# Kernel tuning notes

Measured on AMD Instinct MI355X. Metric: run time of the kernel, lower is better.

Reference implementation:

```python
import jax, jax.numpy as jnp
import numpy as np

N = 100000   # nodes (polyline vectors)
E = 800000   # directed edges (intra-polyline, avg degree 8)
NC = 10000   # clusters (polylines)
C0 = 64      # in_channels
H = 64       # hidden_unit
L = 3        # num_subgraph_layres
LN_EPS = 1e-5


def setup_inputs() -> dict:
    key = jax.random.key(0)
    ks = jax.random.split(key, 4 + 2 * L)
    d = {}
    d["x"] = jax.random.normal(ks[0], (N, C0), jnp.float32)
    d["edge_index"] = jax.random.randint(ks[1], (2, E), 0, N, dtype=jnp.int32)
    d["cluster"] = jax.random.randint(ks[2], (N,), 0, NC, dtype=jnp.int32)
    c = C0
    for i in range(L):
        k1, k2 = jax.random.split(ks[3 + i], 2)
        d[f"W1_{i}"] = jax.random.normal(k1, (c, H), jnp.float32) * (1.0 / np.sqrt(c))
        d[f"b1_{i}"] = jnp.zeros((H,), jnp.float32)
        d[f"g_{i}"] = jnp.ones((H,), jnp.float32)
        d[f"be_{i}"] = jnp.zeros((H,), jnp.float32)
        d[f"W2_{i}"] = jax.random.normal(k2, (H, c), jnp.float32) * (1.0 / np.sqrt(H))
        d[f"b2_{i}"] = jnp.zeros((c,), jnp.float32)
        c *= 2
    return d


def _glp_layer(x, edge_index, W1, b1, g, be, W2, b2):
    # MLP: Linear -> LayerNorm -> ReLU -> Linear
    h = x @ W1 + b1                                   # [N, H]
    mu = h.mean(axis=-1, keepdims=True)
    var = ((h - mu) ** 2).mean(axis=-1, keepdims=True)
    h = (h - mu) * jax.lax.rsqrt(var + LN_EPS) * g + be
    h = jax.nn.relu(h)
    h = h @ W2 + b2                                   # [N, C]
    # message = x_j (source features), aggr='max' at target nodes
    msg = h[edge_index[0]]                            # [E, C] gather
    aggr = jax.ops.segment_max(msg, edge_index[1], num_segments=h.shape[0])
    aggr = jnp.where(jnp.isfinite(aggr), aggr, 0.0)   # nodes with no in-edges -> 0
    # update: concat([x, aggr_out]) -> channels double
    return jnp.concatenate([h, aggr], axis=1)


def reference(x, edge_index, cluster,
              W1_0, b1_0, g_0, be_0, W2_0, b2_0,
              W1_1, b1_1, g_1, be_1, W2_1, b2_1,
              W1_2, b1_2, g_2, be_2, W2_2, b2_2):
    params = [
        (W1_0, b1_0, g_0, be_0, W2_0, b2_0),
        (W1_1, b1_1, g_1, be_1, W2_1, b2_1),
        (W1_2, b1_2, g_2, be_2, W2_2, b2_2),
    ]
    for p in params:
        x = _glp_layer(x, edge_index, *p)
    # max_pool over clusters (per-polyline max)
    pooled = jax.ops.segment_max(x, cluster, num_segments=NC)  # [NC, 8*C0]
    pooled = jnp.where(jnp.isfinite(pooled), pooled, 0.0)
    # column-wise L2 normalization: out.x / out.x.norm(dim=0)
    return pooled / jnp.linalg.norm(pooled, axis=0)
```

## Files before the change

### kernel.cpp

```cpp
#include <hip/hip_runtime.h>
#include <hip/hip_bf16.h>

#define NN 100000
#define NE 800000
#define NCL 10000
#define CAPN 32
#define CAPC 40

typedef __attribute__((ext_vector_type(8))) short short8;
typedef __attribute__((ext_vector_type(4))) float f32x4;

__device__ __forceinline__ float bflo(unsigned int u) {
  return __uint_as_float(u << 16);
}
__device__ __forceinline__ float bfhi(unsigned int u) {
  return __uint_as_float(u & 0xffff0000u);
}
__device__ __forceinline__ unsigned short f2bf(float f) {
  unsigned int u = __float_as_uint(f);
  u += 0x7fffu + ((u >> 16) & 1u);
  return (unsigned short)(u >> 16);
}
__device__ __forceinline__ unsigned int packbf_exact(float lo, float hi) {
  return (__float_as_uint(lo) >> 16) | (__float_as_uint(hi) & 0xffff0000u);
}

struct WtDesc { const float* src; unsigned short* dst; int rows, cols; };
struct WtPack { WtDesc d[6]; };
__global__ __launch_bounds__(256) void prep_kernel(int* zbase, int zn, int zblocks, WtPack p) {
  if ((int)blockIdx.x < zblocks) {
    int i = blockIdx.x * 256 + threadIdx.x;
    if (i < zn) zbase[i] = 0;
    return;
  }
  int b = blockIdx.x - zblocks;
  const long stride = 32L * 256;
  for (int a = 0; a < 6; ++a) {
    int rows = p.d[a].rows, cols = p.d[a].cols, n = rows * cols;
    const float* src = p.d[a].src;
    unsigned short* dst = p.d[a].dst;
    for (long i = (long)b * 256 + threadIdx.x; i < n; i += stride) {
      int r = (int)(i / cols), c = (int)(i % cols);
      dst[(long)c * rows + r] = f2bf(src[(long)r * cols + c]);
    }
  }
}

__device__ __forceinline__ void scatter_body(
    int i,
    const int* __restrict__ ei, int* __restrict__ cnt, int* __restrict__ bucket,
    const int* __restrict__ cl, int* __restrict__ ccnt, int* __restrict__ cbucket) {
  if (i < NE / 4) {
    int4 t = reinterpret_cast<const int4*>(ei + NE)[i];
    int4 s = reinterpret_cast<const int4*>(ei)[i];
    int p0 = atomicAdd(&cnt[t.x], 1);
    int p1 = atomicAdd(&cnt[t.y], 1);
    int p2 = atomicAdd(&cnt[t.z], 1);
    int p3 = atomicAdd(&cnt[t.w], 1);
    if (p0 < CAPN) bucket[t.x * CAPN + p0] = s.x;
    if (p1 < CAPN) bucket[t.y * CAPN + p1] = s.y;
    if (p2 < CAPN) bucket[t.z * CAPN + p2] = s.z;
    if (p3 < CAPN) bucket[t.w * CAPN + p3] = s.w;
  } else if (i < NE / 4 + NN / 4) {
    int j = i - NE / 4;
    int4 c = reinterpret_cast<const int4*>(cl)[j];
    int n0 = j * 4;
    int p0 = atomicAdd(&ccnt[c.x], 1);
    int p1 = atomicAdd(&ccnt[c.y], 1);
    int p2 = atomicAdd(&ccnt[c.z], 1);
    int p3 = atomicAdd(&ccnt[c.w], 1);
    if (p0 < CAPC) cbucket[c.x * CAPC + p0] = n0;
    if (p1 < CAPC) cbucket[c.y * CAPC + p1] = n0 + 1;
    if (p2 < CAPC) cbucket[c.z * CAPC + p2] = n0 + 2;
    if (p3 < CAPC) cbucket[c.w * CAPC + p3] = n0 + 3;
  }
}

template<int C, bool INF32, bool DO_SCATTER>
__global__ __launch_bounds__(256) void mlp_mfma_kernel(
    const void* __restrict__ xin_v,
    const unsigned short* __restrict__ W1T,
    const float* __restrict__ b1, const float* __restrict__ g, const float* __restrict__ be,
    const unsigned short* __restrict__ W2T,
    const float* __restrict__ b2,
    unsigned short* __restrict__ out, int outstride, int ntiles,
    int sblocks,
    const int* __restrict__ ei, int* __restrict__ cnt, int* __restrict__ bucket,
    const int* __restrict__ cl, int* __restrict__ ccnt, int* __restrict__ cbucket)
{
  constexpr int CP = C + 8;
  __shared__ unsigned short w1s[64 * CP];
  __shared__ unsigned short w2s[C * 72];
  __shared__ unsigned short ps[4 * 16 * 72];
  int tid = threadIdx.x;

  if constexpr (DO_SCATTER) {
    if ((int)blockIdx.x < sblocks) {
      scatter_body(blockIdx.x * 256 + tid, ei, cnt, bucket, cl, ccnt, cbucket);
      return;
    }
  }
  int bid = blockIdx.x - (DO_SCATTER ? sblocks : 0);
  int mgrid = gridDim.x - (DO_SCATTER ? sblocks : 0);

  for (int i = tid; i < 64 * (C / 8); i += 256) {
    int r = i / (C / 8), cc = i % (C / 8);
    *reinterpret_cast<uint4*>(&w1s[r * CP + cc * 8]) =
        *reinterpret_cast<const uint4*>(W1T + r * C + cc * 8);
  }
  for (int i = tid; i < C * 8; i += 256) {
    int r = i / 8, cc = i % 8;
    *reinterpret_cast<uint4*>(&w2s[r * 72 + cc * 8]) =
        *reinterpret_cast<const uint4*>(W2T + r * 64 + cc * 8);
  }
  __syncthreads();

  int wv = tid >> 6, lane = tid & 63;
  int l15 = lane & 15, q = lane >> 4;
  unsigned short* psw = &ps[wv * 16 * 72];

  float b1v[4], gv[4], bev[4];
  #pragma unroll
  for (int t = 0; t < 4; ++t) {
    b1v[t] = b1[t * 16 + l15];
    gv[t]  = g[t * 16 + l15];
    bev[t] = be[t * 16 + l15];
  }
  constexpr int NT2 = C / 16;
  float b2v[NT2];
  #pragma unroll
  for (int tc = 0; tc < NT2; ++tc) b2v[tc] = b2[tc * 16 + l15];

  for (long tile = (long)bid * 4 + wv; tile < ntiles; tile += (long)mgrid * 4) {
    long nb = tile * 16;
    long arow = nb + l15;

    f32x4 acc[4];
    #pragma unroll
    for (int t = 0; t < 4; ++t) acc[t] = (f32x4){0.f, 0.f, 0.f, 0.f};
    #pragma unroll
    for (int kk = 0; kk < C / 32; ++kk) {
      short8 a;
      if constexpr (INF32) {
        const float* xf = (const float*)xin_v;
        const float* src = xf + arow * C + kk * 32 + q * 8;
        float4 v0 = reinterpret_cast<const float4*>(src)[0];
        float4 v1 = reinterpret_cast<const float4*>(src)[1];
        a[0] = (short)f2bf(v0.x); a[1] = (short)f2bf(v0.y);
        a[2] = (short)f2bf(v0.z); a[3] = (short)f2bf(v0.w);
        a[4] = (short)f2bf(v1.x); a[5] = (short)f2bf(v1.y);
        a[6] = (short)f2bf(v1.z); a[7] = (short)f2bf(v1.w);
      } else {
        const unsigned short* xh = (const unsigned short*)xin_v;
        a = *reinterpret_cast<const short8*>(xh + arow * C + kk * 32 + q * 8);
      }
      #pragma unroll
      for (int t = 0; t < 4; ++t) {
        short8 b = *reinterpret_cast<const short8*>(&w1s[(t * 16 + l15) * CP + kk * 32 + q * 8]);
        acc[t] = __builtin_amdgcn_mfma_f32_16x16x32_bf16(a, b, acc[t], 0, 0, 0);
      }
    }

    float vout[4][4];
    #pragma unroll
    for (int r = 0; r < 4; ++r) {
      float h0 = acc[0][r] + b1v[0];
      float h1 = acc[1][r] + b1v[1];
      float h2 = acc[2][r] + b1v[2];
      float h3 = acc[3][r] + b1v[3];
      float s = (h0 + h1) + (h2 + h3);
      s += __shfl_xor(s, 1); s += __shfl_xor(s, 2);
      s += __shfl_xor(s, 4); s += __shfl_xor(s, 8);
      float mu = s * (1.0f / 64.0f);
      float d0 = h0 - mu, d1 = h1 - mu, d2 = h2 - mu, d3 = h3 - mu;
      float qs = (d0 * d0 + d1 * d1) + (d2 * d2 + d3 * d3);
      qs += __shfl_xor(qs, 1); qs += __shfl_xor(qs, 2);
      qs += __shfl_xor(qs, 4); qs += __shfl_xor(qs, 8);
      float rinv = rsqrtf(qs * (1.0f / 64.0f) + 1e-5f);
      vout[0][r] = fmaxf(0.f, d0 * rinv * gv[0] + bev[0]);
      vout[1][r] = fmaxf(0.f, d1 * rinv * gv[1] + bev[1]);
      vout[2][r] = fmaxf(0.f, d2 * rinv * gv[2] + bev[2]);
      vout[3][r] = fmaxf(0.f, d3 * rinv * gv[3] + bev[3]);
    }

    #pragma unroll
    for (int t = 0; t < 4; ++t)
      #pragma unroll
      for (int r = 0; r < 4; ++r)
        psw[(q * 4 + r) * 72 + t * 16 + l15] = f2bf(vout[t][r]);

    short8 a0 = *reinterpret_cast<const short8*>(&psw[l15 * 72 + q * 8]);
    short8 a1 = *reinterpret_cast<const short8*>(&psw[l15 * 72 + 32 + q * 8]);
    long node0 = nb + q * 4;
    #pragma unroll
    for (int tc = 0; tc < NT2; ++tc) {
      short8 b0 = *reinterpret_cast<const short8*>(&w2s[(tc * 16 + l15) * 72 + q * 8]);
      short8 b1w = *reinterpret_cast<const short8*>(&w2s[(tc * 16 + l15) * 72 + 32 + q * 8]);
      f32x4 c = (f32x4){0.f, 0.f, 0.f, 0.f};
      c = __builtin_amdgcn_mfma_f32_16x16x32_bf16(a0, b0, c, 0, 0, 0);
      c = __builtin_amdgcn_mfma_f32_16x16x32_bf16(a1, b1w, c, 0, 0, 0);
      #pragma unroll
      for (int r = 0; r < 4; ++r)
        out[(node0 + r) * (long)outstride + tc * 16 + l15] = f2bf(c[r] + b2v[tc]);
    }
  }
}

template<int C>
__global__ __launch_bounds__(256) void aggr_kernel(
    const int* __restrict__ cnt, const int* __restrict__ bucket,
    unsigned short* __restrict__ xnext)
{
  constexpr int Q = C / 8;
  constexpr int NPB = 256 / Q;
  int q = threadIdx.x & (Q - 1);
  int ln = threadIdx.x / Q;
  long node = (long)blockIdx.x * NPB + ln;
  int end = min(cnt[node], CAPN);
  const int* bl = bucket + node * CAPN;
  float m[8];
  #pragma unroll
  for (int k = 0; k < 8; ++k) m[k] = -3.4e38f;

  auto acc8 = [&](uint4 u) {
    m[0] = fmaxf(m[0], bflo(u.x)); m[1] = fmaxf(m[1], bfhi(u.x));
    m[2] = fmaxf(m[2], bflo(u.y)); m[3] = fmaxf(m[3], bfhi(u.y));
    m[4] = fmaxf(m[4], bflo(u.z)); m[5] = fmaxf(m[5], bfhi(u.z));
    m[6] = fmaxf(m[6], bflo(u.w)); m[7] = fmaxf(m[7], bfhi(u.w));
  };
  auto row = [&](int s) {
    return reinterpret_cast<const uint4*>(xnext + (long)s * (2 * C))[q];
  };

  int e = 0;
  for (; e + 3 < end; e += 4) {
    int s0 = bl[e], s1 = bl[e + 1], s2 = bl[e + 2], s3 = bl[e + 3];
    uint4 u0 = row(s0), u1 = row(s1), u2 = row(s2), u3 = row(s3);
    acc8(u0); acc8(u1); acc8(u2); acc8(u3);
  }
  for (; e < end; ++e) acc8(row(bl[e]));
  if (end == 0) {
    #pragma unroll
    for (int k = 0; k < 8; ++k) m[k] = 0.f;
  }
  uint4 o;
  o.x = packbf_exact(m[0], m[1]);
  o.y = packbf_exact(m[2], m[3]);
  o.z = packbf_exact(m[4], m[5]);
  o.w = packbf_exact(m[6], m[7]);
  reinterpret_cast<uint4*>(xnext + (long)node * (2 * C) + C)[q] = o;
}

__global__ __launch_bounds__(256) void pool_kernel(
    const int* __restrict__ ccnt, const int* __restrict__ cbucket,
    const unsigned short* __restrict__ x3, float* __restrict__ pooled)
{
  int q = threadIdx.x & 63;
  int lc = threadIdx.x >> 6;
  long k = (long)blockIdx.x * 4 + lc;
  int end = min(ccnt[k], CAPC);
  const int* bl = cbucket + k * CAPC;
  float m[8];
  #pragma unroll
  for (int t = 0; t < 8; ++t) m[t] = -3.4e38f;

  auto acc8 = [&](uint4 u) {
    m[0] = fmaxf(m[0], bflo(u.x)); m[1] = fmaxf(m[1], bfhi(u.x));
    m[2] = fmaxf(m[2], bflo(u.y)); m[3] = fmaxf(m[3], bfhi(u.y));
    m[4] = fmaxf(m[4], bflo(u.z)); m[5] = fmaxf(m[5], bfhi(u.z));
    m[6] = fmaxf(m[6], bflo(u.w)); m[7] = fmaxf(m[7], bfhi(u.w));
  };
  auto row = [&](int n) {
    return reinterpret_cast<const uint4*>(x3 + (long)n * 512)[q];
  };

  int e = 0;
  for (; e + 3 < end; e += 4) {
    int n0 = bl[e], n1 = bl[e + 1], n2 = bl[e + 2], n3 = bl[e + 3];
    uint4 u0 = row(n0), u1 = row(n1), u2 = row(n2), u3 = row(n3);
    acc8(u0); acc8(u1); acc8(u2); acc8(u3);
  }
  for (; e < end; ++e) acc8(row(bl[e]));
  if (end == 0) {
    #pragma unroll
    for (int t = 0; t < 8; ++t) m[t] = 0.f;
  }
  float* orow = pooled + k * 512 + q * 8;
  reinterpret_cast<float4*>(orow)[0] = make_float4(m[0], m[1], m[2], m[3]);
  reinterpret_cast<float4*>(orow)[1] = make_float4(m[4], m[5], m[6], m[7]);
}

__global__ __launch_bounds__(256) void colnorm_kernel(const float* __restrict__ pooled,
                                                      float* __restrict__ normsq) {
  int tid = threadIdx.x;
  int rows_per = (NCL + gridDim.x - 1) / gridDim.x;
  int r0 = blockIdx.x * rows_per;
  int r1 = min(r0 + rows_per, NCL);
  float s0 = 0.f, s1 = 0.f;
  for (int r = r0; r < r1; ++r) {
    float a = pooled[(long)r * 512 + tid];
    float b = pooled[(long)r * 512 + 256 + tid];
    s0 = fmaf(a, a, s0);
    s1 = fmaf(b, b, s1);
  }
  atomicAdd(&normsq[tid], s0);
  atomicAdd(&normsq[tid + 256], s1);
}

__global__ __launch_bounds__(256) void normalize_kernel(const float* __restrict__ pooled,
                                                        const float* __restrict__ normsq,
                                                        float* __restrict__ out) {
  long idx = (long)blockIdx.x * 256 + threadIdx.x;
  if (idx < (long)NCL * 512) {
    float nv = normsq[idx & 511];
    out[idx] = pooled[idx] * rsqrtf(nv);
  }
}

extern "C" void kernel_launch(void* const* d_in, const int* in_sizes, int n_in,
                              void* d_out, int out_size, void* d_ws, size_t ws_size,
                              hipStream_t stream) {
  const float* x0 = (const float*)d_in[0];
  const int* ei = (const int*)d_in[1];
  const int* cl = (const int*)d_in[2];

  const float* W1f[3]; const float* b1f[3]; const float* gf[3];
  const float* bef[3]; const float* W2f[3]; const float* b2f[3];
  for (int i = 0; i < 3; ++i) {
    W1f[i] = (const float*)d_in[3 + 6 * i + 0];
    b1f[i] = (const float*)d_in[3 + 6 * i + 1];
    gf[i]  = (const float*)d_in[3 + 6 * i + 2];
    bef[i] = (const float*)d_in[3 + 6 * i + 3];
    W2f[i] = (const float*)d_in[3 + 6 * i + 4];
    b2f[i] = (const float*)d_in[3 + 6 * i + 5];
  }

  char* ws = (char*)d_ws;
  size_t off = 0;
  auto take = [&](size_t bytes) {
    size_t o = off; off = (off + bytes + 255) & ~(size_t)255; return o;
  };
  unsigned short* x3 = (unsigned short*)(ws + take((size_t)NN * 512 * 2));
  unsigned short* x1 = x3;
  unsigned short* x2 = (unsigned short*)(ws + take((size_t)NN * 256 * 2));
  size_t szBucket = (size_t)NN * CAPN * 4;
  size_t szPooled = (size_t)NCL * 512 * 4;
  size_t regA = take(szBucket > szPooled ? szBucket : szPooled);
  int* bucket = (int*)(ws + regA);
  float* pooled = (float*)(ws + regA);
  int* cbucket = (int*)(ws + take((size_t)NCL * CAPC * 4));
  int* zero_base = (int*)(ws + take((size_t)(NN + NCL + 512) * 4));
  int* cnt = zero_base;
  int* ccnt = zero_base + NN;
  float* normsq = (float*)(zero_base + NN + NCL);

  int Cs[3] = {64, 128, 256};
  unsigned short *W1T[3], *W2T[3];
  for (int i = 0; i < 3; ++i) {
    W1T[i] = (unsigned short*)(ws + take((size_t)64 * Cs[i] * 2));
    W2T[i] = (unsigned short*)(ws + take((size_t)Cs[i] * 64 * 2));
  }

  if (off > ws_size) return;

  WtPack wp;
  for (int i = 0; i < 3; ++i) {
    wp.d[2 * i + 0] = { W1f[i], W1T[i], Cs[i], 64 };
    wp.d[2 * i + 1] = { W2f[i], W2T[i], 64, Cs[i] };
  }

  int zn = NN + NCL + 512;
  int zblocks = (zn + 255) / 256;
  prep_kernel<<<zblocks + 32, 256, 0, stream>>>(zero_base, zn, zblocks, wp);

  int ntiles = NN / 16;
  int nblk = (ntiles / 2 + 3) / 4;
  int nwork = NE / 4 + NN / 4;
  int sblocks = (nwork + 255) / 256;

  mlp_mfma_kernel<64, true, true><<<sblocks + nblk, 256, 0, stream>>>(
      x0, W1T[0], b1f[0], gf[0], bef[0], W2T[0], b2f[0], x1, 128, ntiles,
      sblocks, ei, cnt, bucket, cl, ccnt, cbucket);
  aggr_kernel<64><<<NN / 32, 256, 0, stream>>>(cnt, bucket, x1);
  mlp_mfma_kernel<128, false, false><<<nblk, 256, 0, stream>>>(
      x1, W1T[1], b1f[1], gf[1], bef[1], W2T[1], b2f[1], x2, 256, ntiles,
      0, nullptr, nullptr, nullptr, nullptr, nullptr, nullptr);
  aggr_kernel<128><<<NN / 16, 256, 0, stream>>>(cnt, bucket, x2);
  mlp_mfma_kernel<256, false, false><<<nblk, 256, 0, stream>>>(
      x2, W1T[2], b1f[2], gf[2], bef[2], W2T[2], b2f[2], x3, 512, ntiles,
      0, nullptr, nullptr, nullptr, nullptr, nullptr, nullptr);
  aggr_kernel<256><<<NN / 8, 256, 0, stream>>>(cnt, bucket, x3);

  pool_kernel<<<NCL / 4, 256, 0, stream>>>(ccnt, cbucket, x3, pooled);
  colnorm_kernel<<<128, 256, 0, stream>>>(pooled, normsq);
  normalize_kernel<<<((long)NCL * 512 + 255) / 256, 256, 0, stream>>>(pooled, normsq, (float*)d_out);
}
```

Baseline: 411.1 us.

## Fuse last-layer edge max-aggregation into cluster pooling kernel

The final layer's neighbor max-aggregation is no longer materialized. The pooling kernel now computes, for each node in a cluster, its max over in-neighbors on the fly and folds it into the right half of the pooled output, while the left half takes the node's own features. This removes the 512-wide x3 write plus its re-read and drops one kernel launch. In exchange the same neighbor gathers run inside a serial per-cluster loop with 32 lanes per cluster, which may lower memory-level parallelism, and the workspace buffers are now aliased differently.

```diff
diff --git a/kernel.cpp b/kernel.cpp
--- a/kernel.cpp
+++ b/kernel.cpp
@@ -251,43 +251,63 @@
   reinterpret_cast<uint4*>(xnext + (long)node * (2 * C) + C)[q] = o;
 }
 
-__global__ __launch_bounds__(256) void pool_kernel(
+__global__ __launch_bounds__(256) void poolfuse_kernel(
     const int* __restrict__ ccnt, const int* __restrict__ cbucket,
-    const unsigned short* __restrict__ x3, float* __restrict__ pooled)
+    const int* __restrict__ cnt, const int* __restrict__ bucket,
+    const unsigned short* __restrict__ h3, float* __restrict__ pooled)
 {
-  int q = threadIdx.x & 63;
-  int lc = threadIdx.x >> 6;
-  long k = (long)blockIdx.x * 4 + lc;
-  int end = min(ccnt[k], CAPC);
-  const int* bl = cbucket + k * CAPC;
-  float m[8];
+  int q = threadIdx.x & 31;
+  int lc = threadIdx.x >> 5;
+  long k = (long)blockIdx.x * 8 + lc;
+  int cend = min(ccnt[k], CAPC);
+  const int* cbl = cbucket + k * CAPC;
+
+  float mL[8], mR[8];
   #pragma unroll
-  for (int t = 0; t < 8; ++t) m[t] = -3.4e38f;
-
-  auto acc8 = [&](uint4 u) {
+  for (int t = 0; t < 8; ++t) { mL[t] = -3.4e38f; mR[t] = -3.4e38f; }
+
+  auto fold = [](float* m, uint4 u) {
     m[0] = fmaxf(m[0], bflo(u.x)); m[1] = fmaxf(m[1], bfhi(u.x));
     m[2] = fmaxf(m[2], bflo(u.y)); m[3] = fmaxf(m[3], bfhi(u.y));
     m[4] = fmaxf(m[4], bflo(u.z)); m[5] = fmaxf(m[5], bfhi(u.z));
     m[6] = fmaxf(m[6], bflo(u.w)); m[7] = fmaxf(m[7], bfhi(u.w));
   };
   auto row = [&](int n) {
-    return reinterpret_cast<const uint4*>(x3 + (long)n * 512)[q];
+    return reinterpret_cast<const uint4*>(h3 + (long)n * 256)[q];
   };
 
-  int e = 0;
-  for (; e + 3 < end; e += 4) {
-    int n0 = bl[e], n1 = bl[e + 1], n2 = bl[e + 2], n3 = bl[e + 3];
-    uint4 u0 = row(n0), u1 = row(n1), u2 = row(n2), u3 = row(n3);
-    acc8(u0); acc8(u1); acc8(u2); acc8(u3);
-  }
-  for (; e < end; ++e) acc8(row(bl[e]));
-  if (end == 0) {
-    #pragma unroll
-    for (int t = 0; t < 8; ++t) m[t] = 0.f;
-  }
-  float* orow = pooled + k * 512 + q * 8;
-  reinterpret_cast<float4*>(orow)[0] = make_float4(m[0], m[1], m[2], m[3]);
-  reinterpret_cast<float4*>(orow)[1] = make_float4(m[4], m[5], m[6], m[7]);
+  for (int i = 0; i < cend; ++i) {
+    int n = cbl[i];
+    fold(mL, row(n));
+    int ee = min(cnt[n], CAPN);
+    const int* bl = bucket + (long)n * CAPN;
+    float nm[8];
+    #pragma unroll
+    for (int t = 0; t < 8; ++t) nm[t] = -3.4e38f;
+    int e = 0;
+    for (; e + 3 < ee; e += 4) {
+      int s0 = bl[e], s1 = bl[e + 1], s2 = bl[e + 2], s3 = bl[e + 3];
+      uint4 u0 = row(s0), u1 = row(s1), u2 = row(s2), u3 = row(s3);
+      fold(nm, u0); fold(nm, u1); fold(nm, u2); fold(nm, u3);
+    }
+    for (; e < ee; ++e) fold(nm, row(bl[e]));
+    if (ee == 0) {
+      #pragma unroll
+      for (int t = 0; t < 8; ++t) nm[t] = 0.f;
+    }
+    #pragma unroll
+    for (int t = 0; t < 8; ++t) mR[t] = fmaxf(mR[t], nm[t]);
+  }
+  if (cend == 0) {
+    #pragma unroll
+    for (int t = 0; t < 8; ++t) { mL[t] = 0.f; mR[t] = 0.f; }
+  }
+  float* oL = pooled + k * 512 + q * 8;
+  float* oR = oL + 256;
+  reinterpret_cast<float4*>(oL)[0] = make_float4(mL[0], mL[1], mL[2], mL[3]);
+  reinterpret_cast<float4*>(oL)[1] = make_float4(mL[4], mL[5], mL[6], mL[7]);
+  reinterpret_cast<float4*>(oR)[0] = make_float4(mR[0], mR[1], mR[2], mR[3]);
+  reinterpret_cast<float4*>(oR)[1] = make_float4(mR[4], mR[5], mR[6], mR[7]);
 }
 
 __global__ __launch_bounds__(256) void colnorm_kernel(const float* __restrict__ pooled,
@@ -340,14 +360,11 @@
   auto take = [&](size_t bytes) {
     size_t o = off; off = (off + bytes + 255) & ~(size_t)255; return o;
   };
-  unsigned short* x3 = (unsigned short*)(ws + take((size_t)NN * 512 * 2));
-  unsigned short* x1 = x3;
+  unsigned short* x1 = (unsigned short*)(ws + take((size_t)NN * 256 * 2));
+  unsigned short* x3c = x1;
   unsigned short* x2 = (unsigned short*)(ws + take((size_t)NN * 256 * 2));
-  size_t szBucket = (size_t)NN * CAPN * 4;
-  size_t szPooled = (size_t)NCL * 512 * 4;
-  size_t regA = take(szBucket > szPooled ? szBucket : szPooled);
-  int* bucket = (int*)(ws + regA);
-  float* pooled = (float*)(ws + regA);
+  float* pooled = (float*)x2;
+  int* bucket = (int*)(ws + take((size_t)NN * CAPN * 4));
   int* cbucket = (int*)(ws + take((size_t)NCL * CAPC * 4));
   int* zero_base = (int*)(ws + take((size_t)(NN + NCL + 512) * 4));
   int* cnt = zero_base;
@@ -387,11 +404,10 @@
       0, nullptr, nullptr, nullptr, nullptr, nullptr, nullptr);
   aggr_kernel<128><<<NN / 16, 256, 0, stream>>>(cnt, bucket, x2);
   mlp_mfma_kernel<256, false, false><<<nblk, 256, 0, stream>>>(
-      x2, W1T[2], b1f[2], gf[2], bef[2], W2T[2], b2f[2], x3, 512, ntiles,
+      x2, W1T[2], b1f[2], gf[2], bef[2], W2T[2], b2f[2], x3c, 256, ntiles,
       0, nullptr, nullptr, nullptr, nullptr, nullptr, nullptr);
-  aggr_kernel<256><<<NN / 8, 256, 0, stream>>>(cnt, bucket, x3);
-
-  pool_kernel<<<NCL / 4, 256, 0, stream>>>(ccnt, cbucket, x3, pooled);
+
+  poolfuse_kernel<<<NCL / 8, 256, 0, stream>>>(ccnt, cbucket, cnt, bucket, x3c, pooled);
   colnorm_kernel<<<128, 256, 0, stream>>>(pooled, normsq);
   normalize_kernel<<<((long)NCL * 512 + 255) / 256, 256, 0, stream>>>(pooled, normsq, (float*)d_out);
 }
```

Measured after the change: 417.0 us. No clear change (+1.4%).
